# Performance work log

Hardware: AMD Instinct MI355X
Metric: run time of the kernel (lower is better)

Reference implementation:

```python
import jax, jax.numpy as jnp
import numpy as np

B, S, D, H, KS, VS, O = 4, 2048, 1024, 16, 64, 64, 1024


def setup_inputs() -> dict:
    key = jax.random.key(0)
    ks = jax.random.split(key, 11)
    def w(k, shp):
        return jax.random.normal(k, shp, dtype=jnp.float32) * 0.02
    return {
        "Q": jax.random.normal(ks[0], (B, S, D), dtype=jnp.float32),
        "K": jax.random.normal(ks[1], (B, S, D), dtype=jnp.float32),
        "V": jax.random.normal(ks[2], (B, S, D), dtype=jnp.float32),
        # per-head projection weights stacked over heads (equivalent to 3*H separate nn.Linear)
        "Wq": w(ks[3], (H, D, KS)), "bq": w(ks[4], (H, KS)),
        "Wk": w(ks[5], (H, D, KS)), "bk": w(ks[6], (H, KS)),
        "Wv": w(ks[7], (H, D, VS)), "bv": w(ks[8], (H, VS)),
        "Wo": w(ks[9], (H * VS, O)), "bo": w(ks[10], (O,)),
    }


def reference(Q, K, V, Wq, bq, Wk, bk, Wv, bv, Wo, bo):
    scale = jnp.sqrt(jnp.asarray(KS, dtype=Q.dtype))
    # per-head linear projections (vectorized over heads)
    q = jnp.einsum('bsd,hdk->bhsk', Q, Wq) + bq[:, None, :]   # [B,H,S,KS]
    k = jnp.einsum('bsd,hdk->bhsk', K, Wk) + bk[:, None, :]   # [B,H,S,KS]
    v = jnp.einsum('bsd,hdv->bhsv', V, Wv) + bv[:, None, :]   # [B,H,S,VS]
    # scaled dot-product attention, full S x S scores per head
    scores = jnp.einsum('bhsk,bhtk->bhst', q, k) / scale       # [B,H,S,S]
    attn = jax.nn.softmax(scores, axis=-1)
    heads = jnp.einsum('bhst,bhtv->bhsv', attn, v)             # [B,H,S,VS]
    # concat heads along feature dim -> [B,S,H*VS]
    cat = jnp.transpose(heads, (0, 2, 1, 3)).reshape(B, S, H * VS)
    return cat @ Wo + bo
```

## Files before the change

kernel.cpp:

```cpp
#include <hip/hip_runtime.h>
#include <hip/hip_fp16.h>
#include <cstdint>
#include <cstddef>

typedef _Float16 f16;
typedef _Float16 f16x8 __attribute__((ext_vector_type(8)));
typedef _Float16 f16x4 __attribute__((ext_vector_type(4)));
typedef float    f32x4 __attribute__((ext_vector_type(4)));

#define MFMA(a, b, c) __builtin_amdgcn_mfma_f32_16x16x32_f16(a, b, c, 0, 0, 0)


__device__ __forceinline__ void gload_lds16(const f16* g, f16* l) {
    __builtin_amdgcn_global_load_lds(
        (const __attribute__((address_space(1))) void*)g,
        (__attribute__((address_space(3))) void*)l, 16, 0, 0);
}

__global__ void k_convert3(const float* __restrict__ Q, const float* __restrict__ K,
                           const float* __restrict__ V, f16* __restrict__ Qh,
                           f16* __restrict__ Kh, f16* __restrict__ Vh) {
    const int seg = blockIdx.x >> 11;
    const int lb  = blockIdx.x & 2047;
    const float* src = seg == 0 ? Q : (seg == 1 ? K : V);
    f16* dst = seg == 0 ? Qh : (seg == 1 ? Kh : Vh);
    int i = lb * blockDim.x + threadIdx.x;
    for (; i < 2097152; i += 524288) {
        float4 v = ((const float4*)src)[i];
        f16x4 h;
        h[0] = (f16)v.x; h[1] = (f16)v.y; h[2] = (f16)v.z; h[3] = (f16)v.w;
        ((f16x4*)dst)[i] = h;
    }
}

__global__ void k_transpose_all(const float* __restrict__ Wq, const float* __restrict__ Wk,
                                const float* __restrict__ Wv, const float* __restrict__ Wo,
                                f16* __restrict__ WT, f16* __restrict__ WoT) {
    __shared__ float T[64][65];
    const int bx = blockIdx.x;
    const int widx = bx >> 8, sub = bx & 255;
    const int nb = sub >> 4, db = sub & 15;
    const int tid = threadIdx.x;
    const float* W = widx == 0 ? Wq : (widx == 1 ? Wk : (widx == 2 ? Wv : Wo));
    f16* Wt = (widx < 3) ? (WT + (size_t)widx * 1048576) : WoT;
    const float* src = (widx < 3) ? (W + nb * 65536 + db * 4096)
                                  : (W + db * 65536 + nb * 64);
    const int rstride = (widx < 3) ? 64 : 1024;
    {
        int nn = tid & 63, d0 = tid >> 6;
#pragma unroll
        for (int p = 0; p < 16; ++p) {
            int dd = p * 4 + d0;
            T[dd][nn] = src[dd * rstride + nn];
        }
    }
    __syncthreads();
    {
        int dd = tid & 63, n0 = tid >> 6;
#pragma unroll
        for (int p = 0; p < 16; ++p) {
            int nn = p * 4 + n0;
            Wt[(size_t)(nb * 64 + nn) * 1024 + db * 64 + dd] = (f16)T[dd][nn];
        }
    }
}

#define G256_STAGE(AD, BD, ASRC, BSRC, KT)                                      \
    do {                                                                        \
        int ktc = (KT);                                                         \
        _Pragma("unroll")                                                       \
        for (int i2 = 0; i2 < 4; ++i2) {                                        \
            int gA = wid * 4 + i2;                                              \
            gload_lds16(&(ASRC)[(size_t)(row0 + gA * 8 + (lane >> 3)) * 1024    \
                                + ktc * 64 + (lane & 7) * 8],                   \
                        &(AD)[(gA * 68 + lane) * 8]);                           \
        }                                                                       \
        _Pragma("unroll")                                                       \
        for (int i2 = 0; i2 < 2; ++i2) {                                        \
            int gB = wid * 2 + i2;                                              \
            gload_lds16(&(BSRC)[(size_t)(col0 + gB * 8 + (lane >> 3)) * 1024    \
                                + ktc * 64 + (lane & 7) * 8],                   \
                        &(BD)[(gB * 68 + lane) * 8]);                           \
        }                                                                       \
    } while (0)

#define G256_COMPUTE(AB, BB)                                                    \
    do {                                                                        \
        _Pragma("unroll")                                                       \
        for (int kk = 0; kk < 2; ++kk) {                                        \
            f16x8 af[4], bf[4];                                                 \
            _Pragma("unroll")                                                   \
            for (int m = 0; m < 4; ++m) {                                       \
                int rw = wm * 64 + m * 16 + lr;                                 \
                af[m] = *(const f16x8*)&(AB)[((rw >> 3) * 68 + (rw & 7) * 8     \
                                              + kk * 4 + lg) * 8];              \
            }                                                                   \
            _Pragma("unroll")                                                   \
            for (int n = 0; n < 4; ++n) {                                       \
                int rw = wn * 64 + n * 16 + lr;                                 \
                bf[n] = *(const f16x8*)&(BB)[((rw >> 3) * 68 + (rw & 7) * 8     \
                                              + kk * 4 + lg) * 8];              \
            }                                                                   \
            _Pragma("unroll")                                                   \
            for (int m = 0; m < 4; ++m)                                         \
                _Pragma("unroll")                                               \
                for (int n = 0; n < 4; ++n)                                     \
                    acc[m][n] = MFMA(af[m], bf[n], acc[m][n]);                  \
        }                                                                       \
    } while (0)

#define G256_PIPELINE(ASRC, BSRC)                                              \
    int cur = 0, nx1 = 1, nx2 = 2;                                             \
    G256_STAGE(As3, Bs3, ASRC, BSRC, 0);                                       \
    for (int t = 0; t < 16; ++t) {                                             \
        int tn = t < 15 ? t + 1 : 15;                                          \
        G256_STAGE(As3 + nx1 * 17408, Bs3 + nx1 * 8704, ASRC, BSRC, tn);       \
        asm volatile("s_waitcnt vmcnt(6)" ::: "memory");                       \
        __builtin_amdgcn_sched_barrier(0);                                     \
        __builtin_amdgcn_s_barrier();                                          \
        __builtin_amdgcn_sched_barrier(0);                                     \
        const f16* Ab = As3 + cur * 17408;                                     \
        const f16* Bb = Bs3 + cur * 8704;                                      \
        G256_COMPUTE(Ab, Bb);                                                  \
        int tmp = cur; cur = nx1; nx1 = nx2; nx2 = tmp;                        \
    }

__global__ __launch_bounds__(512, 1) void k_gemm_qkv256(
    const f16* __restrict__ Qh, const f16* __restrict__ Kh, const f16* __restrict__ Vh,
    const f16* __restrict__ WT, const float* __restrict__ bq,
    const float* __restrict__ bk, const float* __restrict__ bv,
    f16* __restrict__ qout, f16* __restrict__ kout, f16* __restrict__ vout, float SC) {
    __shared__ f16 As3[3 * 17408];
    __shared__ f16 Bs3[3 * 8704];
    const int yy = blockIdx.y;
    const int seg = yy >> 3;
    const f16* A    = seg == 0 ? Qh : (seg == 1 ? Kh : Vh);
    const f16* Bt   = WT + (size_t)seg * 1048576;
    const float* bias = seg == 0 ? bq : (seg == 1 ? bk : bv);
    const float scale = seg == 0 ? SC : 1.0f;

    const int tid = threadIdx.x;
    const int wid = tid >> 6, lane = tid & 63;
    const int wm = wid >> 1, wn = wid & 1;
    const int lr = lane & 15, lg = lane >> 4;
    const int row0 = blockIdx.x * 256, col0 = (yy & 7) * 128;

    f32x4 acc[4][4];
#pragma unroll
    for (int m = 0; m < 4; ++m)
#pragma unroll
        for (int n = 0; n < 4; ++n) acc[m][n] = (f32x4){0.f, 0.f, 0.f, 0.f};

    G256_PIPELINE(A, Bt)

#pragma unroll
    for (int m = 0; m < 4; ++m) {
#pragma unroll
        for (int n = 0; n < 4; ++n) {
            int col = col0 + wn * 64 + n * 16 + lr;
            float bv_ = bias[col];
            int rowb = row0 + wm * 64 + m * 16 + lg * 4;
            int srow = rowb & 2047;
            if (seg == 0) {
#pragma unroll
                for (int r = 0; r < 4; ++r) {
                    int row = rowb + r;
                    size_t a = ((size_t)((row >> 11) * 16 + (col >> 6)) * 2048 + (row & 2047)) * 64 + (col & 63);
                    qout[a] = (f16)((acc[m][n][r] + bv_) * scale);
                }
            } else if (seg == 1) {
                int ks5 = srow & 31;
                int p0 = ((ks5 >> 2) & 1) * 16 + (ks5 >> 3) * 4 + (ks5 & 3);
                size_t abase = (size_t)((rowb >> 11) * 16 + (col >> 6)) * 131072
                             + (size_t)(srow >> 5) * 2048
                             + (size_t)(p0 >> 4) * 512
                             + (size_t)((col & 63) >> 5) * 1024
                             + (size_t)((col & 31) >> 3) * 128
                             + (col & 7);
#pragma unroll
                for (int r = 0; r < 4; ++r)
                    kout[abase + (size_t)((p0 & 15) + r) * 8] = (f16)(acc[m][n][r] + bv_);
            } else {
                size_t a = (size_t)((rowb >> 11) * 16 + (col >> 6)) * 131072
                         + (size_t)(srow >> 5) * 2048
                         + (size_t)((col & 63) >> 4) * 512
                         + (size_t)((srow & 31) >> 3) * 128
                         + (size_t)(col & 15) * 8
                         + (srow & 7);
                f16x4 ov;
#pragma unroll
                for (int r = 0; r < 4; ++r) ov[r] = (f16)(acc[m][n][r] + bv_);
                *(f16x4*)&vout[a] = ov;
            }
        }
    }
}

__global__ __launch_bounds__(512, 1) void k_gemm_out256(const f16* __restrict__ A,
                                                        const f16* __restrict__ Bt,
                                                        const float* __restrict__ bias,
                                                        float* __restrict__ Cout) {
    __shared__ f16 As3[3 * 17408];
    __shared__ f16 Bs3[3 * 8704];
    const int tid = threadIdx.x;
    const int wid = tid >> 6, lane = tid & 63;
    const int wm = wid >> 1, wn = wid & 1;
    const int lr = lane & 15, lg = lane >> 4;
    const int row0 = blockIdx.x * 256, col0 = blockIdx.y * 128;

    f32x4 acc[4][4];
#pragma unroll
    for (int m = 0; m < 4; ++m)
#pragma unroll
        for (int n = 0; n < 4; ++n) acc[m][n] = (f32x4){0.f, 0.f, 0.f, 0.f};

    G256_PIPELINE(A, Bt)

#pragma unroll
    for (int m = 0; m < 4; ++m) {
#pragma unroll
        for (int n = 0; n < 4; ++n) {
            int col = col0 + wn * 64 + n * 16 + lr;
            float bv = bias[col];
#pragma unroll
            for (int r = 0; r < 4; ++r) {
                int row = row0 + wm * 64 + m * 16 + lg * 4 + r;
                Cout[(size_t)row * 1024 + col] = acc[m][n][r] + bv;
            }
        }
    }
}

#define ATTN_TILE(Kc, Vc)                                                     \
    do {                                                                      \
        f16x8 ka0 = *(const f16x8*)&(Kc)[fo];                                 \
        f16x8 ka1 = *(const f16x8*)&(Kc)[fo + 1024];                          \
        f16x8 ka2 = *(const f16x8*)&(Kc)[fo + 512];                           \
        f16x8 ka3 = *(const f16x8*)&(Kc)[fo + 1536];                          \
        f32x4 st[2][2];                                                       \
        __builtin_amdgcn_s_setprio(1);                                        \
        _Pragma("unroll")                                                     \
        for (int qt = 0; qt < 2; ++qt) {                                      \
            float nm = -m_r[qt];                                              \
            f32x4 z = (f32x4){nm, nm, nm, nm};                                \
            z = MFMA(ka0, qf[qt][0], z);                                      \
            z = MFMA(ka1, qf[qt][1], z);                                      \
            st[qt][0] = z;                                                    \
            f32x4 z2 = (f32x4){nm, nm, nm, nm};                               \
            z2 = MFMA(ka2, qf[qt][0], z2);                                    \
            z2 = MFMA(ka3, qf[qt][1], z2);                                    \
            st[qt][1] = z2;                                                   \
        }                                                                     \
        __builtin_amdgcn_s_setprio(0);                                        \
        f16x8 vv0 = *(const f16x8*)&(Vc)[fo];                                 \
        f16x8 vv1 = *(const f16x8*)&(Vc)[fo + 512];                           \
        f16x8 vv2 = *(const f16x8*)&(Vc)[fo + 1024];                          \
        f16x8 vv3 = *(const f16x8*)&(Vc)[fo + 1536];                          \
        {                                                                     \
            float lm[2];                                                      \
            _Pragma("unroll")                                                 \
            for (int qt = 0; qt < 2; ++qt) {                                  \
                float a0 = fmaxf(fmaxf(st[qt][0][0], st[qt][0][1]), st[qt][0][2]); \
                float b0 = fmaxf(fmaxf(st[qt][0][3], st[qt][1][0]), st[qt][1][1]); \
                float c0 = fmaxf(fmaxf(st[qt][1][2], st[qt][1][3]), a0);      \
                lm[qt] = fmaxf(b0, c0);                                       \
            }                                                                 \
            if (__any((lm[0] > THR) || (lm[1] > THR))) {                      \
                _Pragma("unroll")                                             \
                for (int qt = 0; qt < 2; ++qt) {                              \
                    float t0v = lm[qt];                                       \
                    t0v = fmaxf(t0v, __shfl_xor(t0v, 16, 64));                \
                    t0v = fmaxf(t0v, __shfl_xor(t0v, 32, 64));                \
                    float delta = fmaxf(0.f, t0v);                            \
                    float alpha = __builtin_amdgcn_exp2f(-delta);             \
                    _Pragma("unroll")                                         \
                    for (int m = 0; m < 4; ++m)                               \
                        _Pragma("unroll")                                     \
                        for (int r = 0; r < 4; ++r) o[qt][m][r] *= alpha;     \
                    _Pragma("unroll")                                         \
                    for (int r = 0; r < 4; ++r) ol[qt][r] *= alpha;           \
                    m_r[qt] += delta;                                         \
                    _Pragma("unroll")                                         \
                    for (int t = 0; t < 2; ++t)                               \
                        _Pragma("unroll")                                     \
                        for (int r = 0; r < 4; ++r) st[qt][t][r] -= delta;    \
                }                                                             \
            }                                                                 \
        }                                                                     \
        f16x8 pf[2];                                                          \
        _Pragma("unroll")                                                     \
        for (int qt = 0; qt < 2; ++qt) {                                      \
            union { uint32_t u[4]; f16x8 v; } bb;                             \
            _Pragma("unroll")                                                 \
            for (int t = 0; t < 2; ++t)                                       \
                _Pragma("unroll")                                             \
                for (int pr = 0; pr < 2; ++pr) {                              \
                    float e0 = __builtin_amdgcn_exp2f(st[qt][t][2 * pr]);     \
                    float e1 = __builtin_amdgcn_exp2f(st[qt][t][2 * pr + 1]); \
                    auto hp = __builtin_amdgcn_cvt_pkrtz(e0, e1);             \
                    bb.u[t * 2 + pr] = __builtin_bit_cast(uint32_t, hp);      \
                }                                                             \
            pf[qt] = bb.v;                                                    \
        }                                                                     \
        __builtin_amdgcn_s_setprio(1);                                        \
        _Pragma("unroll")                                                     \
        for (int qt = 0; qt < 2; ++qt) {                                      \
            o[qt][0] = MFMA(vv0, pf[qt], o[qt][0]);                           \
            o[qt][1] = MFMA(vv1, pf[qt], o[qt][1]);                           \
            o[qt][2] = MFMA(vv2, pf[qt], o[qt][2]);                           \
            o[qt][3] = MFMA(vv3, pf[qt], o[qt][3]);                           \
            ol[qt]   = MFMA(ones, pf[qt], ol[qt]);                            \
        }                                                                     \
        __builtin_amdgcn_s_setprio(0);                                        \
    } while (0)

__global__ __launch_bounds__(512, 4) void k_attn(const f16* __restrict__ q,
                                                 const f16* __restrict__ k2,
                                                 const f16* __restrict__ v2,
                                                 f16* __restrict__ cat) {
    const int g = blockIdx.x;
    const int xcd = g & 7, i = g >> 3;
    const int bh = xcd * 8 + (i >> 3);
    const int qb = i & 7;
    const int b = bh >> 4, h = bh & 15;

    const int tid = threadIdx.x, wid = tid >> 6, lane = tid & 63;
    const int lr = lane & 15, lg = lane >> 4;
    const int qw = qb * 256 + wid * 32;

    __shared__ f16 Ks[4][2048];
    __shared__ f16 Vs[4][2048];

    const float THR = 8.0f;

    f16x8 qf[2][2];
#pragma unroll
    for (int qt = 0; qt < 2; ++qt)
#pragma unroll
        for (int hf = 0; hf < 2; ++hf)
            qf[qt][hf] = *(const f16x8*)&q[((size_t)bh * 2048 + qw + qt * 16 + lr) * 64 + hf * 32 + lg * 8];

    const f16* kt = k2 + (size_t)bh * 131072;
    const f16* vt = v2 + (size_t)bh * 131072;
    const bool sgK = (tid < 256);
    const int so2 = (tid & 255) * 8;
    const int fo = lane * 8;

    f16x8 ones;
#pragma unroll
    for (int j = 0; j < 8; ++j) ones[j] = (f16)1.0f;

    f32x4 o[2][4], ol[2];
#pragma unroll
    for (int qt = 0; qt < 2; ++qt) {
#pragma unroll
        for (int m = 0; m < 4; ++m) o[qt][m] = (f32x4){0.f, 0.f, 0.f, 0.f};
        ol[qt] = (f32x4){0.f, 0.f, 0.f, 0.f};
    }
    float m_r[2] = {0.f, 0.f};

    if (sgK) {
        gload_lds16(kt + so2, &Ks[0][so2]);
        gload_lds16(kt + 2048 + so2, &Ks[1][so2]);
    } else {
        gload_lds16(vt + so2, &Vs[0][so2]);
        gload_lds16(vt + 2048 + so2, &Vs[1][so2]);
    }
    __syncthreads();

    const bool rev = (wid & 1);
    for (int pp = 0; pp < 32; ++pp) {
        const int t0 = 2 * pp;
        const int ba = t0 & 3, bb2 = (t0 + 1) & 3;
        const int bc = (t0 + 2) & 3, bd = (t0 + 3) & 3;

        if (sgK) {
            gload_lds16(kt + (size_t)(t0 + 2) * 2048 + so2, &Ks[bc][so2]);
            gload_lds16(kt + (size_t)(t0 + 3) * 2048 + so2, &Ks[bd][so2]);
        } else {
            gload_lds16(vt + (size_t)(t0 + 2) * 2048 + so2, &Vs[bc][so2]);
            gload_lds16(vt + (size_t)(t0 + 3) * 2048 + so2, &Vs[bd][so2]);
        }

        if (rev) {
            ATTN_TILE(&Ks[bb2][0], &Vs[bb2][0]);
            ATTN_TILE(&Ks[ba][0], &Vs[ba][0]);
        } else {
            ATTN_TILE(&Ks[ba][0], &Vs[ba][0]);
            ATTN_TILE(&Ks[bb2][0], &Vs[bb2][0]);
        }

        __syncthreads();
    }

#pragma unroll
    for (int qt = 0; qt < 2; ++qt) {
        float inv = 1.f / ol[qt][0];
        size_t cb = ((size_t)b * 2048 + qw + qt * 16 + lr) * 1024 + h * 64 + lg * 4;
#pragma unroll
        for (int m = 0; m < 4; ++m) {
            f16x4 ov;
#pragma unroll
            for (int r = 0; r < 4; ++r) ov[r] = (f16)(o[qt][m][r] * inv);
            *(f16x4*)&cat[cb + m * 16] = ov;
        }
    }
}

extern "C" void kernel_launch(void* const* d_in, const int* in_sizes, int n_in,
                              void* d_out, int out_size, void* d_ws, size_t ws_size,
                              hipStream_t stream) {
    const float* Q  = (const float*)d_in[0];
    const float* K  = (const float*)d_in[1];
    const float* V  = (const float*)d_in[2];
    const float* Wq = (const float*)d_in[3];
    const float* bq = (const float*)d_in[4];
    const float* Wk = (const float*)d_in[5];
    const float* bk = (const float*)d_in[6];
    const float* Wv = (const float*)d_in[7];
    const float* bv = (const float*)d_in[8];
    const float* Wo = (const float*)d_in[9];
    const float* bo = (const float*)d_in[10];

    char* ws = (char*)d_ws;
    size_t off = 0;
    auto alloc = [&](size_t bytes) {
        char* p = ws + off;
        off += (bytes + 255) & ~(size_t)255;
        return p;
    };
    f16* Qh  = (f16*)alloc(8192ULL * 1024 * 2);
    f16* Kh  = (f16*)alloc(8192ULL * 1024 * 2);
    f16* Vh  = (f16*)alloc(8192ULL * 1024 * 2);
    f16* WT  = (f16*)alloc(3ULL * 1024 * 1024 * 2);
    f16* WoT = (f16*)alloc(1024ULL * 1024 * 2);
    f16* qb  = (f16*)alloc(8192ULL * 1024 * 2);
    f16* kb2 = (f16*)alloc(8192ULL * 1024 * 2);
    f16* vb2 = (f16*)alloc(8192ULL * 1024 * 2);
    f16* cat = (f16*)alloc(8192ULL * 1024 * 2);

    k_convert3<<<6144, 256, 0, stream>>>(Q, K, V, Qh, Kh, Vh);
    k_transpose_all<<<1024, 256, 0, stream>>>(Wq, Wk, Wv, Wo, WT, WoT);

    const float SC = 0.125f * 1.44269504089f;
    k_gemm_qkv256<<<dim3(32, 24), 512, 0, stream>>>(Qh, Kh, Vh, WT, bq, bk, bv,
                                                    qb, kb2, vb2, SC);

    k_attn<<<512, 512, 0, stream>>>(qb, kb2, vb2, cat);

    k_gemm_out256<<<dim3(32, 8), 512, 0, stream>>>(cat, WoT, bo, (float*)d_out);
}
```

Measured before the change: 190.2 us.

## Fuse fp32-to-fp16 input conversion into QKV projection GEMM loads

Drops the separate conversion kernel for Q, K and V and has the QKV GEMM read fp32 activations directly. It converts them to fp16 in registers with packed convert instructions before writing them to LDS. This removes a full extra pass writing and re-reading half-precision copies of the inputs. In exchange, A tiles now travel through registers with synchronous waits instead of async direct-to-LDS loads, and the GEMM reads twice as many bytes per A tile.

Measured after the change: 183.4 us. 1.04x faster.

```diff
diff --git a/kernel.cpp b/kernel.cpp
--- a/kernel.cpp
+++ b/kernel.cpp
@@ -15,22 +15,6 @@
     __builtin_amdgcn_global_load_lds(
         (const __attribute__((address_space(1))) void*)g,
         (__attribute__((address_space(3))) void*)l, 16, 0, 0);
-}
-
-__global__ void k_convert3(const float* __restrict__ Q, const float* __restrict__ K,
-                           const float* __restrict__ V, f16* __restrict__ Qh,
-                           f16* __restrict__ Kh, f16* __restrict__ Vh) {
-    const int seg = blockIdx.x >> 11;
-    const int lb  = blockIdx.x & 2047;
-    const float* src = seg == 0 ? Q : (seg == 1 ? K : V);
-    f16* dst = seg == 0 ? Qh : (seg == 1 ? Kh : Vh);
-    int i = lb * blockDim.x + threadIdx.x;
-    for (; i < 2097152; i += 524288) {
-        float4 v = ((const float4*)src)[i];
-        f16x4 h;
-        h[0] = (f16)v.x; h[1] = (f16)v.y; h[2] = (f16)v.z; h[3] = (f16)v.w;
-        ((f16x4*)dst)[i] = h;
-    }
 }
 
 __global__ void k_transpose_all(const float* __restrict__ Wq, const float* __restrict__ Wk,
@@ -81,6 +65,49 @@
             gload_lds16(&(BSRC)[(size_t)(col0 + gB * 8 + (lane >> 3)) * 1024    \
                                 + ktc * 64 + (lane & 7) * 8],                   \
                         &(BD)[(gB * 68 + lane) * 8]);                           \
+        }                                                                       \
+    } while (0)
+
+#define G256_STAGE_B(BD, BSRC, KT)                                             \
+    do {                                                                        \
+        int ktc = (KT);                                                         \
+        _Pragma("unroll")                                                       \
+        for (int i2 = 0; i2 < 2; ++i2) {                                        \
+            int gB = wid * 2 + i2;                                              \
+            gload_lds16(&(BSRC)[(size_t)(col0 + gB * 8 + (lane >> 3)) * 1024    \
+                                + ktc * 64 + (lane & 7) * 8],                   \
+                        &(BD)[(gB * 68 + lane) * 8]);                           \
+        }                                                                       \
+    } while (0)
+
+#define QKV_ISSUE_A(KT)                                                         \
+    do {                                                                        \
+        int ktc = (KT);                                                         \
+        _Pragma("unroll")                                                       \
+        for (int i2 = 0; i2 < 4; ++i2) {                                        \
+            int gA = wid * 4 + i2;                                              \
+            const float* p = &Af[(size_t)(row0 + gA * 8 + (lane >> 3)) * 1024   \
+                                 + ktc * 64 + (lane & 7) * 8];                  \
+            alo[i2] = *(const float4*)p;                                        \
+            ahi[i2] = *(const float4*)(p + 4);                                  \
+        }                                                                       \
+    } while (0)
+
+#define QKV_WRITE_A(AD)                                                         \
+    do {                                                                        \
+        _Pragma("unroll")                                                       \
+        for (int i2 = 0; i2 < 4; ++i2) {                                        \
+            int gA = wid * 4 + i2;                                              \
+            union { uint32_t u[4]; f16x8 v; } hh;                               \
+            hh.u[0] = __builtin_bit_cast(uint32_t,                              \
+                        __builtin_amdgcn_cvt_pkrtz(alo[i2].x, alo[i2].y));      \
+            hh.u[1] = __builtin_bit_cast(uint32_t,                              \
+                        __builtin_amdgcn_cvt_pkrtz(alo[i2].z, alo[i2].w));      \
+            hh.u[2] = __builtin_bit_cast(uint32_t,                              \
+                        __builtin_amdgcn_cvt_pkrtz(ahi[i2].x, ahi[i2].y));      \
+            hh.u[3] = __builtin_bit_cast(uint32_t,                              \
+                        __builtin_amdgcn_cvt_pkrtz(ahi[i2].z, ahi[i2].w));      \
+            *(f16x8*)&(AD)[(gA * 68 + lane) * 8] = hh.v;                        \
         }                                                                       \
     } while (0)
 
@@ -126,7 +153,7 @@
     }
 
 __global__ __launch_bounds__(512, 1) void k_gemm_qkv256(
-    const f16* __restrict__ Qh, const f16* __restrict__ Kh, const f16* __restrict__ Vh,
+    const float* __restrict__ Qf, const float* __restrict__ Kf, const float* __restrict__ Vf,
     const f16* __restrict__ WT, const float* __restrict__ bq,
     const float* __restrict__ bk, const float* __restrict__ bv,
     f16* __restrict__ qout, f16* __restrict__ kout, f16* __restrict__ vout, float SC) {
@@ -134,7 +161,7 @@
     __shared__ f16 Bs3[3 * 8704];
     const int yy = blockIdx.y;
     const int seg = yy >> 3;
-    const f16* A    = seg == 0 ? Qh : (seg == 1 ? Kh : Vh);
+    const float* Af = seg == 0 ? Qf : (seg == 1 ? Kf : Vf);
     const f16* Bt   = WT + (size_t)seg * 1048576;
     const float* bias = seg == 0 ? bq : (seg == 1 ? bk : bv);
     const float scale = seg == 0 ? SC : 1.0f;
@@ -151,7 +178,36 @@
 #pragma unroll
         for (int n = 0; n < 4; ++n) acc[m][n] = (f32x4){0.f, 0.f, 0.f, 0.f};
 
-    G256_PIPELINE(A, Bt)
+    float4 alo[4], ahi[4];
+
+    G256_STAGE_B(Bs3, Bt, 0);
+    QKV_ISSUE_A(0);
+    asm volatile("s_waitcnt vmcnt(0)" ::: "memory");
+    QKV_WRITE_A(As3);
+    G256_STAGE_B(Bs3 + 8704, Bt, 1);
+    QKV_ISSUE_A(1);
+    asm volatile("s_waitcnt lgkmcnt(0)" ::: "memory");
+    __builtin_amdgcn_sched_barrier(0);
+    __builtin_amdgcn_s_barrier();
+    __builtin_amdgcn_sched_barrier(0);
+
+    int cur = 0, nx1 = 1, nx2 = 2;
+    for (int t = 0; t < 16; ++t) {
+        const f16* Ab = As3 + cur * 17408;
+        const f16* Bb = Bs3 + cur * 8704;
+        G256_COMPUTE(Ab, Bb);
+        int tn2 = t + 2 <= 15 ? t + 2 : 15;
+        asm volatile("s_waitcnt vmcnt(0)" ::: "memory");
+        __builtin_amdgcn_sched_barrier(0);
+        QKV_WRITE_A(As3 + nx1 * 17408);
+        G256_STAGE_B(Bs3 + nx2 * 8704, Bt, tn2);
+        QKV_ISSUE_A(tn2);
+        asm volatile("s_waitcnt lgkmcnt(0)" ::: "memory");
+        __builtin_amdgcn_sched_barrier(0);
+        __builtin_amdgcn_s_barrier();
+        __builtin_amdgcn_sched_barrier(0);
+        int tmp = cur; cur = nx1; nx1 = nx2; nx2 = tmp;
+    }
 
 #pragma unroll
     for (int m = 0; m < 4; ++m) {
@@ -429,9 +485,6 @@
         off += (bytes + 255) & ~(size_t)255;
         return p;
     };
-    f16* Qh  = (f16*)alloc(8192ULL * 1024 * 2);
-    f16* Kh  = (f16*)alloc(8192ULL * 1024 * 2);
-    f16* Vh  = (f16*)alloc(8192ULL * 1024 * 2);
     f16* WT  = (f16*)alloc(3ULL * 1024 * 1024 * 2);
     f16* WoT = (f16*)alloc(1024ULL * 1024 * 2);
     f16* qb  = (f16*)alloc(8192ULL * 1024 * 2);
@@ -439,11 +492,10 @@
     f16* vb2 = (f16*)alloc(8192ULL * 1024 * 2);
     f16* cat = (f16*)alloc(8192ULL * 1024 * 2);
 
-    k_convert3<<<6144, 256, 0, stream>>>(Q, K, V, Qh, Kh, Vh);
     k_transpose_all<<<1024, 256, 0, stream>>>(Wq, Wk, Wv, Wo, WT, WoT);
 
     const float SC = 0.125f * 1.44269504089f;
-    k_gemm_qkv256<<<dim3(32, 24), 512, 0, stream>>>(Qh, Kh, Vh, WT, bq, bk, bv,
+    k_gemm_qkv256<<<dim3(32, 24), 512, 0, stream>>>(Q, K, V, WT, bq, bk, bv,
                                                     qb, kb2, vb2, SC);
 
     k_attn<<<512, 512, 0, stream>>>(qb, kb2, vb2, cat);
```
